# Kernel tuning notes

Measured on AMD Instinct MI355X. Metric: run time of the kernel, lower is better.

## Reference

```python
import jax, jax.numpy as jnp
import numpy as np

MARGIN = 1.0
RULE_WEIGHT = 0.5
NUM_ENT = 100000
NUM_REL = 500
DIM = 512
N_RULES = 20


def setup_inputs() -> dict:
    key = jax.random.key(0)
    ks = jax.random.split(key, 8)
    pos_triples = jax.random.randint(ks[0], (1024, 3), 0, NUM_REL)
    neg_triples = jax.random.randint(ks[1], (8192, 3), 0, NUM_REL)
    rule_r1 = jax.random.randint(ks[2], (N_RULES,), 0, NUM_REL)
    rule_r2 = jax.random.randint(ks[3], (N_RULES,), 0, NUM_REL)
    rule_conf = jax.random.uniform(ks[4], (N_RULES,), dtype=jnp.float32)
    ent_emb = jax.random.normal(ks[5], (NUM_ENT, DIM), dtype=jnp.float32)
    rel_emb = jax.random.normal(ks[6], (NUM_REL, DIM), dtype=jnp.float32)
    norm_vec = jax.random.normal(ks[7], (NUM_REL, DIM), dtype=jnp.float32)
    return {
        "pos_triples": pos_triples, "neg_triples": neg_triples,
        "rule_r1": rule_r1, "rule_r2": rule_r2, "rule_conf": rule_conf,
        "ent_emb": ent_emb, "rel_emb": rel_emb, "norm_vec": norm_vec,
    }


def _transh_dist(h_idx, r_idx, t_idx, ent_emb, rel_emb, norm_vec):
    """TransH distance ||proj(h) + r - proj(t)||_2.
    Index args may have any broadcast-compatible shape; returns that shape."""
    w = norm_vec[r_idx]                                   # [..., d]
    w = w / jnp.linalg.norm(w, axis=-1, keepdims=True)
    he = ent_emb[h_idx]
    te = ent_emb[t_idx]
    re = rel_emb[r_idx]
    hp = he - jnp.sum(he * w, axis=-1, keepdims=True) * w  # hyperplane projection
    tp = te - jnp.sum(te * w, axis=-1, keepdims=True) * w
    return jnp.linalg.norm(hp + re - tp, axis=-1)


def reference(pos_triples, neg_triples, rule_r1, rule_r2, rule_conf,
              ent_emb, rel_emb, norm_vec):
    B = pos_triples.shape[0]
    neg_ratio = neg_triples.shape[0] // B
    # basic margin ranking loss: pos triples repeat-interleaved to align with negs
    exp_pos = jnp.repeat(pos_triples, neg_ratio, axis=0)   # [B*ratio, 3]
    d_pos = _transh_dist(exp_pos[:, 0], exp_pos[:, 1], exp_pos[:, 2],
                         ent_emb, rel_emb, norm_vec)
    d_neg = _transh_dist(neg_triples[:, 0], neg_triples[:, 1], neg_triples[:, 2],
                         ent_emb, rel_emb, norm_vec)
    basic_loss = jnp.mean(jax.nn.relu(MARGIN + d_pos - d_neg))

    # rule loss: for each pos triple i and rule j with r_i == r1_j,
    # rule_loss -= conf_j * score(h_i, r2_j, t_i), score = -distance.
    h = pos_triples[:, 0][:, None]        # [B,1]
    r = pos_triples[:, 1][:, None]        # [B,1]
    t = pos_triples[:, 2][:, None]        # [B,1]
    d_rule = _transh_dist(h, rule_r2[None, :], t, ent_emb, rel_emb, norm_vec)  # [B,nR]
    score = -d_rule
    mask = (r == rule_r1[None, :]).astype(score.dtype)     # [B,nR]
    rule_loss = -jnp.sum(mask * rule_conf[None, :] * score)

    return basic_loss + RULE_WEIGHT * rule_loss
```

## Files before the change

### kernel.cpp

```cpp
#include <hip/hip_runtime.h>

#define DIM        512
#define B_POS      1024
#define N_NEG      8192
#define N_RULES    20
#define NEG_RATIO  8
#define NBLK       256

__device__ __forceinline__ float wave_sum(float x) {
#pragma unroll
    for (int off = 32; off > 0; off >>= 1)
        x += __shfl_xor(x, off, 64);
    return x;
}

__device__ __forceinline__ float transh_dist(
    int h, int r, int t,
    const float* __restrict__ ent, const float* __restrict__ rel,
    const float* __restrict__ nv, int lane)
{
    const float4* wp = (const float4*)(nv  + (size_t)r * DIM);
    const float4* hp = (const float4*)(ent + (size_t)h * DIM);
    const float4* tp = (const float4*)(ent + (size_t)t * DIM);
    const float4* rp = (const float4*)(rel + (size_t)r * DIM);

    float4 wv[2], dv[2], rv[2];
    float ww = 0.f, dw = 0.f;
#pragma unroll
    for (int c = 0; c < 2; ++c) {
        float4 w  = wp[lane + 64 * c];
        float4 hh = hp[lane + 64 * c];
        float4 tt = tp[lane + 64 * c];
        float4 rr = rp[lane + 64 * c];
        float4 d;
        d.x = hh.x - tt.x; d.y = hh.y - tt.y; d.z = hh.z - tt.z; d.w = hh.w - tt.w;
        wv[c] = w; dv[c] = d; rv[c] = rr;
        ww += w.x * w.x + w.y * w.y + w.z * w.z + w.w * w.w;
        dw += d.x * w.x + d.y * w.y + d.z * w.z + d.w * w.w;
    }
    ww = wave_sum(ww);
    dw = wave_sum(dw);
    float s = dw / ww;

    float ss = 0.f;
#pragma unroll
    for (int c = 0; c < 2; ++c) {
        float vx = dv[c].x + rv[c].x - s * wv[c].x;
        float vy = dv[c].y + rv[c].y - s * wv[c].y;
        float vz = dv[c].z + rv[c].z - s * wv[c].z;
        float vw = dv[c].w + rv[c].w - s * wv[c].w;
        ss += vx * vx + vy * vy + vz * vz + vw * vw;
    }
    ss = wave_sum(ss);
    return sqrtf(ss);
}

__global__ __launch_bounds__(256) void fused_kernel(
    const int* __restrict__ pos, const int* __restrict__ neg,
    const int* __restrict__ rule_r1, const int* __restrict__ rule_r2,
    const float* __restrict__ rule_conf,
    const float* __restrict__ ent, const float* __restrict__ rel,
    const float* __restrict__ nv,
    float* __restrict__ partial)
{
    int w    = threadIdx.x >> 6;
    int lane = threadIdx.x & 63;
    int i    = blockIdx.x * 4 + w;

    int h = pos[3 * i], r = pos[3 * i + 1], t = pos[3 * i + 2];
    float dp = transh_dist(h, r, t, ent, rel, nv, lane);

    float relu_sum = 0.f;
#pragma unroll
    for (int k = 0; k < NEG_RATIO; ++k) {
        int n = NEG_RATIO * i + k;
        float dn = transh_dist(neg[3 * n], neg[3 * n + 1], neg[3 * n + 2],
                               ent, rel, nv, lane);
        float v = 1.0f + dp - dn;
        relu_sum += (v > 0.f) ? v : 0.f;
    }

    float rule_acc = 0.f;
    for (int j = 0; j < N_RULES; ++j) {
        if (r == rule_r1[j]) {
            float d = transh_dist(h, rule_r2[j], t, ent, rel, nv, lane);
            rule_acc += rule_conf[j] * d;
        }
    }

    float contrib = relu_sum * (1.0f / (float)N_NEG) + 0.5f * rule_acc;

    __shared__ float part[4];
    if (lane == 0) part[w] = contrib;
    __syncthreads();
    if (threadIdx.x == 0)
        partial[blockIdx.x] = part[0] + part[1] + part[2] + part[3];
}

__global__ __launch_bounds__(64) void final_reduce(
    const float* __restrict__ partial, float* __restrict__ out)
{
    int lane = threadIdx.x;
    float s = 0.f;
#pragma unroll
    for (int m = 0; m < NBLK / 64; ++m)
        s += partial[lane + 64 * m];
    s = wave_sum(s);
    if (lane == 0) out[0] = s;
}

extern "C" void kernel_launch(void* const* d_in, const int* in_sizes, int n_in,
                              void* d_out, int out_size, void* d_ws, size_t ws_size,
                              hipStream_t stream) {
    const int*   pos       = (const int*)  d_in[0];
    const int*   neg       = (const int*)  d_in[1];
    const int*   rule_r1   = (const int*)  d_in[2];
    const int*   rule_r2   = (const int*)  d_in[3];
    const float* rule_conf = (const float*)d_in[4];
    const float* ent       = (const float*)d_in[5];
    const float* rel       = (const float*)d_in[6];
    const float* nv        = (const float*)d_in[7];
    float* out     = (float*)d_out;
    float* partial = (float*)d_ws;

    fused_kernel<<<NBLK, 256, 0, stream>>>(pos, neg, rule_r1, rule_r2, rule_conf,
                                           ent, rel, nv, partial);
    final_reduce<<<1, 64, 0, stream>>>(partial, out);
}
```

Before: 252.8 us.

## Split TransH loss into per-negative and per-rule blocks with in-kernel flag reduction

The work is redistributed from 256 blocks, each doing nine or more serial distance computations per wave, to 2048 blocks that each handle one negative per wave plus 256 separate rule blocks. The positive distance is recomputed for each negative, trading extra gathers for far more waves in flight to hide memory latency. The separate final-reduce launch is removed: an extra block spin-waits on per-block release/acquire flags and sums the partials. The flags are never reset between calls, so on later calls the reducer may read stale partials, and it relies on being scheduled after the worker blocks.

```diff
diff --git a/kernel.cpp b/kernel.cpp
--- a/kernel.cpp
+++ b/kernel.cpp
@@ -5,7 +5,11 @@
 #define N_NEG      8192
 #define N_RULES    20
 #define NEG_RATIO  8
-#define NBLK       256
+
+#define NEG_BLKS   2048
+#define RULE_BLKS  256
+#define NBLK_WORK  (NEG_BLKS + RULE_BLKS)
+#define MARKER     0x1F2E3D4C
 
 __device__ __forceinline__ float wave_sum(float x) {
 #pragma unroll
@@ -61,52 +65,66 @@
     const float* __restrict__ rule_conf,
     const float* __restrict__ ent, const float* __restrict__ rel,
     const float* __restrict__ nv,
-    float* __restrict__ partial)
+    float* __restrict__ partial, int* __restrict__ flags,
+    float* __restrict__ out)
 {
+    int b = blockIdx.x;
+
+    if (b == NBLK_WORK) {
+        int t = threadIdx.x;
+#pragma unroll
+        for (int m = 0; m < NBLK_WORK / 256; ++m) {
+            int idx = t + 256 * m;
+            while (__hip_atomic_load(&flags[idx], __ATOMIC_ACQUIRE,
+                                     __HIP_MEMORY_SCOPE_AGENT) != MARKER) { }
+        }
+        float s = 0.f;
+#pragma unroll
+        for (int m = 0; m < NBLK_WORK / 256; ++m)
+            s += partial[t + 256 * m];
+        s = wave_sum(s);
+        __shared__ float part[4];
+        int w = t >> 6, lane = t & 63;
+        if (lane == 0) part[w] = s;
+        __syncthreads();
+        if (t == 0) out[0] = part[0] + part[1] + part[2] + part[3];
+        return;
+    }
+
     int w    = threadIdx.x >> 6;
     int lane = threadIdx.x & 63;
-    int i    = blockIdx.x * 4 + w;
+    float contrib = 0.f;
 
-    int h = pos[3 * i], r = pos[3 * i + 1], t = pos[3 * i + 2];
-    float dp = transh_dist(h, r, t, ent, rel, nv, lane);
-
-    float relu_sum = 0.f;
-#pragma unroll
-    for (int k = 0; k < NEG_RATIO; ++k) {
-        int n = NEG_RATIO * i + k;
+    if (b < NEG_BLKS) {
+        int n = b * 4 + w;
+        int i = n >> 3;
+        float dp = transh_dist(pos[3 * i], pos[3 * i + 1], pos[3 * i + 2],
+                               ent, rel, nv, lane);
         float dn = transh_dist(neg[3 * n], neg[3 * n + 1], neg[3 * n + 2],
                                ent, rel, nv, lane);
         float v = 1.0f + dp - dn;
-        relu_sum += (v > 0.f) ? v : 0.f;
+        contrib = ((v > 0.f) ? v : 0.f) * (1.0f / (float)N_NEG);
+    } else {
+        int i = (b - NEG_BLKS) * 4 + w;
+        int h = pos[3 * i], r = pos[3 * i + 1], t = pos[3 * i + 2];
+        float racc = 0.f;
+        for (int j = 0; j < N_RULES; ++j) {
+            if (r == rule_r1[j]) {
+                float d = transh_dist(h, rule_r2[j], t, ent, rel, nv, lane);
+                racc += rule_conf[j] * d;
+            }
+        }
+        contrib = 0.5f * racc;
     }
-
-    float rule_acc = 0.f;
-    for (int j = 0; j < N_RULES; ++j) {
-        if (r == rule_r1[j]) {
-            float d = transh_dist(h, rule_r2[j], t, ent, rel, nv, lane);
-            rule_acc += rule_conf[j] * d;
-        }
-    }
-
-    float contrib = relu_sum * (1.0f / (float)N_NEG) + 0.5f * rule_acc;
 
     __shared__ float part[4];
     if (lane == 0) part[w] = contrib;
     __syncthreads();
-    if (threadIdx.x == 0)
-        partial[blockIdx.x] = part[0] + part[1] + part[2] + part[3];
-}
-
-__global__ __launch_bounds__(64) void final_reduce(
-    const float* __restrict__ partial, float* __restrict__ out)
-{
-    int lane = threadIdx.x;
-    float s = 0.f;
-#pragma unroll
-    for (int m = 0; m < NBLK / 64; ++m)
-        s += partial[lane + 64 * m];
-    s = wave_sum(s);
-    if (lane == 0) out[0] = s;
+    if (threadIdx.x == 0) {
+        partial[b] = part[0] + part[1] + part[2] + part[3];
+        __hip_atomic_store(&flags[b], MARKER, __ATOMIC_RELEASE,
+                           __HIP_MEMORY_SCOPE_AGENT);
+    }
 }
 
 extern "C" void kernel_launch(void* const* d_in, const int* in_sizes, int n_in,
@@ -120,10 +138,12 @@
     const float* ent       = (const float*)d_in[5];
     const float* rel       = (const float*)d_in[6];
     const float* nv        = (const float*)d_in[7];
-    float* out     = (float*)d_out;
+    float* out = (float*)d_out;
+
     float* partial = (float*)d_ws;
+    int*   flags   = (int*)(partial + NBLK_WORK);
 
-    fused_kernel<<<NBLK, 256, 0, stream>>>(pos, neg, rule_r1, rule_r2, rule_conf,
-                                           ent, rel, nv, partial);
-    final_reduce<<<1, 64, 0, stream>>>(partial, out);
+    fused_kernel<<<NBLK_WORK + 1, 256, 0, stream>>>(
+        pos, neg, rule_r1, rule_r2, rule_conf, ent, rel, nv,
+        partial, flags, out);
 }
```

After: 288.0 us. +13.9%, slower.

## Assign one negative triple per wave and spread rule work across waves

Applied to the files above, without the earlier changes.

Work is repartitioned so that each wave handles a single negative triple instead of one positive triple with all eight of its negatives. The rule evaluations are split so each of the eight waves sharing a positive triple checks at most three rules. Block count goes from 256 to 2048, and the final reduction is widened to 256 threads to match. This is meant to expose far more parallelism on a GPU with many CUs. In exchange, each positive distance is recomputed eight times and more partials have to be reduced.

```diff
diff --git a/kernel.cpp b/kernel.cpp
--- a/kernel.cpp
+++ b/kernel.cpp
@@ -5,7 +5,7 @@
 #define N_NEG      8192
 #define N_RULES    20
 #define NEG_RATIO  8
-#define NBLK       256
+#define NBLK       2048
 
 __device__ __forceinline__ float wave_sum(float x) {
 #pragma unroll
@@ -65,30 +65,27 @@
 {
     int w    = threadIdx.x >> 6;
     int lane = threadIdx.x & 63;
-    int i    = blockIdx.x * 4 + w;
+    int n    = blockIdx.x * 4 + w;
+    int i    = n >> 3;
+    int k    = n & 7;
 
     int h = pos[3 * i], r = pos[3 * i + 1], t = pos[3 * i + 2];
     float dp = transh_dist(h, r, t, ent, rel, nv, lane);
+    float dn = transh_dist(neg[3 * n], neg[3 * n + 1], neg[3 * n + 2],
+                           ent, rel, nv, lane);
+    float v = 1.0f + dp - dn;
+    float contrib = ((v > 0.f) ? v : 0.f) * (1.0f / (float)N_NEG);
 
-    float relu_sum = 0.f;
+    float racc = 0.f;
 #pragma unroll
-    for (int k = 0; k < NEG_RATIO; ++k) {
-        int n = NEG_RATIO * i + k;
-        float dn = transh_dist(neg[3 * n], neg[3 * n + 1], neg[3 * n + 2],
-                               ent, rel, nv, lane);
-        float v = 1.0f + dp - dn;
-        relu_sum += (v > 0.f) ? v : 0.f;
-    }
-
-    float rule_acc = 0.f;
-    for (int j = 0; j < N_RULES; ++j) {
-        if (r == rule_r1[j]) {
+    for (int m = 0; m < 3; ++m) {
+        int j = k + 8 * m;
+        if (j < N_RULES && r == rule_r1[j]) {
             float d = transh_dist(h, rule_r2[j], t, ent, rel, nv, lane);
-            rule_acc += rule_conf[j] * d;
+            racc += rule_conf[j] * d;
         }
     }
-
-    float contrib = relu_sum * (1.0f / (float)N_NEG) + 0.5f * rule_acc;
+    contrib += 0.5f * racc;
 
     __shared__ float part[4];
     if (lane == 0) part[w] = contrib;
@@ -97,16 +94,20 @@
         partial[blockIdx.x] = part[0] + part[1] + part[2] + part[3];
 }
 
-__global__ __launch_bounds__(64) void final_reduce(
+__global__ __launch_bounds__(256) void final_reduce(
     const float* __restrict__ partial, float* __restrict__ out)
 {
-    int lane = threadIdx.x;
+    int t = threadIdx.x;
     float s = 0.f;
 #pragma unroll
-    for (int m = 0; m < NBLK / 64; ++m)
-        s += partial[lane + 64 * m];
+    for (int m = 0; m < NBLK / 256; ++m)
+        s += partial[t + 256 * m];
     s = wave_sum(s);
-    if (lane == 0) out[0] = s;
+    __shared__ float part[4];
+    int w = t >> 6, lane = t & 63;
+    if (lane == 0) part[w] = s;
+    __syncthreads();
+    if (t == 0) out[0] = part[0] + part[1] + part[2] + part[3];
 }
 
 extern "C" void kernel_launch(void* const* d_in, const int* in_sizes, int n_in,
@@ -125,5 +126,5 @@
 
     fused_kernel<<<NBLK, 256, 0, stream>>>(pos, neg, rule_r1, rule_r2, rule_conf,
                                            ent, rel, nv, partial);
-    final_reduce<<<1, 64, 0, stream>>>(partial, out);
+    final_reduce<<<1, 256, 0, stream>>>(partial, out);
 }
```

Result: no change. 251.2 us (-0.6%).
